# Kernel tuning notes

Measured on AMD Instinct MI355X. Metric: run time of the kernel, lower is better.

The kernel has to match this reference:

```python
import jax, jax.numpy as jnp
import numpy as np

B, T, V, H = 1, 1024, 32000, 2048
NH, NKV, HD = 8, 4, 256
QS, KVS = NH * HD, NKV * HD
I, L = 8192, 2
SCALE = 256.0 ** -0.5          # query_pre_attn_scalar ** -0.5
ATTN_CAP, FINAL_CAP = 50.0, 30.0
WIN, EPS, THETA = 512, 1e-6, 10000.0
NEG = -2.3819763e38


def setup_inputs() -> dict:
    key = jax.random.key(0)
    ks = jax.random.split(key, 12)
    s = 0.02
    return {
        "tokens": jax.random.randint(ks[0], (B, T), 0, V, dtype=jnp.int32),
        "embed": jax.random.normal(ks[1], (V, H), jnp.float32) * s,
        "qkv_w": jax.random.normal(ks[2], (L, (NH + 2 * NKV) * HD, H), jnp.float32) * s,
        "o_w": jax.random.normal(ks[3], (L, H, NH * HD), jnp.float32) * s,
        "gate_w": jax.random.normal(ks[4], (L, I, H), jnp.float32) * s,
        "up_w": jax.random.normal(ks[5], (L, I, H), jnp.float32) * s,
        "down_w": jax.random.normal(ks[6], (L, H, I), jnp.float32) * s,
        "ln_in": jax.random.normal(ks[7], (L, H), jnp.float32) * s,   # RMSNorm weight (zeros-init offset)
        "ln_pa": jax.random.normal(ks[8], (L, H), jnp.float32) * s,
        "ln_pre": jax.random.normal(ks[9], (L, H), jnp.float32) * s,
        "ln_post": jax.random.normal(ks[10], (L, H), jnp.float32) * s,
        "ln_f": jax.random.normal(ks[11], (H,), jnp.float32) * s,
    }


def rmsnorm(x, w):
    x = x.astype(jnp.float32)
    n = x * jax.lax.rsqrt(jnp.mean(x * x, axis=-1, keepdims=True) + EPS)
    return n * (1.0 + w)  # add_unit_offset=True


def rope(x, cos, sin):
    # x: [B, T, N, HD]; split-half complex rotary as in apply_rotary_emb
    x1, x2 = jnp.split(x, 2, axis=-1)
    c = cos[None, :, None, :]
    s = sin[None, :, None, :]
    return jnp.concatenate([x1 * c - x2 * s, x1 * s + x2 * c], axis=-1)


def reference(tokens, embed, qkv_w, o_w, gate_w, up_w, down_w,
              ln_in, ln_pa, ln_pre, ln_post, ln_f):
    pos = jnp.arange(T)
    inv = 1.0 / (THETA ** (jnp.arange(0, HD, 2, dtype=jnp.float32) / HD))  # [HD/2]
    ang = pos.astype(jnp.float32)[:, None] * inv[None, :]
    cos, sin = jnp.cos(ang), jnp.sin(ang)

    i, j = pos[:, None], pos[None, :]
    causal = j <= i
    mask_global = jnp.where(causal, 0.0, NEG).astype(jnp.float32)
    mask_local = jnp.where(causal & (i - j < WIN), 0.0, NEG).astype(jnp.float32)
    masks = [mask_local, mask_global]  # layer 0: LOCAL_SLIDING, layer 1: GLOBAL

    x = embed[tokens] * jnp.sqrt(jnp.float32(H))  # Gemma embedding normalizer

    for l in range(L):
        h = rmsnorm(x, ln_in[l])
        qkv = jnp.einsum('bth,oh->bto', h, qkv_w[l])
        q = qkv[..., :QS].reshape(B, T, NH, HD)
        k = qkv[..., QS:QS + KVS].reshape(B, T, NKV, HD)
        v = qkv[..., QS + KVS:].reshape(B, T, NKV, HD)
        q = rope(q, cos, sin)
        k = rope(k, cos, sin)
        # prefill: kv_write_indices=arange(T) -> cache == current k/v
        k = jnp.repeat(k, NH // NKV, axis=2)  # GQA repeat_interleave over heads
        v = jnp.repeat(v, NH // NKV, axis=2)
        scores = jnp.einsum('bqhd,bkhd->bhqk', q * SCALE, k)
        scores = jnp.tanh(scores / ATTN_CAP) * ATTN_CAP
        scores = scores + masks[l][None, None]
        attn = jax.nn.softmax(scores.astype(jnp.float32), axis=-1)
        out = jnp.einsum('bhqk,bkhd->bqhd', attn, v).reshape(B, T, NH * HD)
        out = jnp.einsum('bto,ho->bth', out, o_w[l])
        x = x + rmsnorm(out, ln_pa[l])

        h = rmsnorm(x, ln_pre[l])
        gate = jax.nn.gelu(jnp.einsum('bth,ih->bti', h, gate_w[l]), approximate=True)
        up = jnp.einsum('bth,ih->bti', h, up_w[l])
        ff = jnp.einsum('bti,hi->bth', gate * up, down_w[l])
        x = x + rmsnorm(ff, ln_post[l])

    x = rmsnorm(x, ln_f)
    logits = jnp.einsum('bth,vh->btv', x, embed)
    logits = jnp.tanh(logits / FINAL_CAP) * FINAL_CAP  # final_logit_softcapping
    return logits
```

## Files before the change

### kernel.cpp

```cpp
#include <hip/hip_runtime.h>
#include <hip/hip_bf16.h>
#include <math.h>

typedef unsigned short u16;
typedef __attribute__((ext_vector_type(8))) short bf16x8;
typedef __attribute__((ext_vector_type(4))) float f32x4;
typedef __attribute__((ext_vector_type(4))) u16 u16x4;
typedef __attribute__((ext_vector_type(4))) unsigned u32x4;

#define T_SEQ 1024
#define HDIM  2048
#define NHEAD 8
#define NKVH  4
#define HSZ   256
#define ISZ   8192
#define NVOC  32000

#define GLDS(src, dst) __builtin_amdgcn_global_load_lds( \
    (const __attribute__((address_space(1))) void*)(src), \
    (__attribute__((address_space(3))) void*)(dst), 16, 0, 0)

__device__ __forceinline__ u16 f2bf(float f) {
    union { float f; unsigned u; } v; v.f = f;
    return (u16)((v.u + 0x7fffu + ((v.u >> 16) & 1u)) >> 16);
}
__device__ __forceinline__ float bf2f(u16 h) {
    union { unsigned u; float f; } v; v.u = (unsigned)h << 16; return v.f;
}

__device__ __forceinline__ unsigned cvt_pk_bf16(float a, float b) {
    unsigned r;
    asm("v_cvt_pk_bf16_f32 %0, %1, %2" : "=v"(r) : "v"(a), "v"(b));
    return r;
}

__device__ __forceinline__ float fast_tanh(float x) {
    float e = __expf(-2.0f * fabsf(x));
    float t = (1.0f - e) / (1.0f + e);
    return copysignf(t, x);
}

__device__ __forceinline__ f32x4 mfma16(bf16x8 a, bf16x8 b, f32x4 c) {
    return __builtin_amdgcn_mfma_f32_16x16x32_bf16(a, b, c, 0, 0, 0);
}

template<int EPI>
__global__ __launch_bounds__(512, 1)
void gemm_f(const u16* __restrict__ A, int lda,
            const float* __restrict__ B, int ldb,
            float* __restrict__ C, int ldc, long sC, int K)
{
    extern __shared__ char lds[];
    const int t = threadIdx.x;
    const int lane = t & 63, wid = t >> 6;
    const int z = blockIdx.z;
    A += (long)z * K;
    B += (long)z * K;
    C += (long)z * sC;

    const int nwg = gridDim.x * gridDim.y;
    int flat = blockIdx.y * gridDim.x + blockIdx.x;
    {
        const int q = nwg >> 3, r = nwg & 7;
        const int xcd = flat & 7, loc = flat >> 3;
        flat = (xcd < r ? xcd * (q + 1) : r * (q + 1) + (xcd - r) * q) + loc;
    }
    const int gm = gridDim.y;
    const long m0 = (long)(flat % gm) * 256;
    const long n0 = (long)(flat / gm) * 128;

    const int ar = t >> 3;
    const int asl = ((t & 7) ^ (ar & 7)) * 8;
    const u16* gA0 = A + (m0 + ar)       * (long)lda + asl;
    const u16* gA1 = A + (m0 + 64 + ar)  * (long)lda + asl;
    const u16* gA2 = A + (m0 + 128 + ar) * (long)lda + asl;
    const u16* gA3 = A + (m0 + 192 + ar) * (long)lda + asl;
    const int br = t >> 4;
    const int bsl = ((t & 15) ^ (br & 15)) * 4;
    const float* gB0 = B + (n0 + br)      * (long)ldb + bsl;
    const float* gB1 = B + (n0 + 32 + br) * (long)ldb + bsl;
    const float* gB2 = B + (n0 + 64 + br) * (long)ldb + bsl;
    const float* gB3 = B + (n0 + 96 + br) * (long)ldb + bsl;

    auto stage = [&](int kt) {
        const long ko = (long)kt * 64;
        char* d = lds + (kt & 1) * 65536 + t * 16;
        GLDS(gA0 + ko, d);
        GLDS(gA1 + ko, d + 8192);
        GLDS(gA2 + ko, d + 16384);
        GLDS(gA3 + ko, d + 24576);
        GLDS(gB0 + ko, d + 32768);
        GLDS(gB1 + ko, d + 40960);
        GLDS(gB2 + ko, d + 49152);
        GLDS(gB3 + ko, d + 57344);
    };

    f32x4 acc[4][4] = {};
    const int fr = lane & 15, kq = lane >> 4;
    const int wm = wid >> 1, wn = wid & 1;
    const int ps0 = ((kq)     ^ (fr & 7)) * 8;
    const int ps1 = ((4 + kq) ^ (fr & 7)) * 8;

    const int KT = K >> 6;
    stage(0);
    stage(1);

    for (int kt = 0; kt < KT; ++kt) {
        if (kt < KT - 1) asm volatile("s_waitcnt vmcnt(8)" ::: "memory");
        else             asm volatile("s_waitcnt vmcnt(0)" ::: "memory");
        __builtin_amdgcn_s_barrier();

        const u16*   As = (const u16*)(lds + (kt & 1) * 65536);
        const float* Bs = (const float*)(lds + (kt & 1) * 65536 + 32768);
        const int arow = wm * 64 + fr;
        const int brow = wn * 64 + fr;

        #pragma unroll
        for (int kk = 0; kk < 2; ++kk) {
            const int ps = kk ? ps1 : ps0;
            const int G = 8 * kk + 2 * kq;
            const int sa = G ^ fr, sb = (G + 1) ^ fr;
            bf16x8 af[4], bfv[4];
            #pragma unroll
            for (int mi = 0; mi < 4; ++mi)
                af[mi] = *(const bf16x8*)(As + (arow + mi * 16) * 64 + ps);
            #pragma unroll
            for (int ni = 0; ni < 4; ++ni) {
                const float* rp = Bs + (brow + ni * 16) * 64;
                f32x4 v0 = *(const f32x4*)(rp + sa * 4);
                f32x4 v1 = *(const f32x4*)(rp + sb * 4);
                u32x4 bw;
                bw.x = cvt_pk_bf16(v0.x, v0.y);
                bw.y = cvt_pk_bf16(v0.z, v0.w);
                bw.z = cvt_pk_bf16(v1.x, v1.y);
                bw.w = cvt_pk_bf16(v1.z, v1.w);
                bfv[ni] = __builtin_bit_cast(bf16x8, bw);
            }
            __builtin_amdgcn_s_setprio(1);
            #pragma unroll
            for (int mi = 0; mi < 4; ++mi)
                #pragma unroll
                for (int ni = 0; ni < 4; ++ni)
                    acc[mi][ni] = mfma16(af[mi], bfv[ni], acc[mi][ni]);
            __builtin_amdgcn_s_setprio(0);
        }
        __builtin_amdgcn_s_barrier();
        if (kt + 2 < KT) stage(kt + 2);
    }

    const int crb = kq * 4, ccol = fr;
    #pragma unroll
    for (int mi = 0; mi < 4; ++mi) {
        #pragma unroll
        for (int rr = 0; rr < 4; ++rr) {
            const long row = m0 + wm * 64 + mi * 16 + crb + rr;
            float* cp = C + row * ldc + n0 + wn * 64 + ccol;
            #pragma unroll
            for (int ni = 0; ni < 4; ++ni) {
                float v = acc[mi][ni][rr];
                if (EPI == 1) v = fast_tanh(v * (1.0f / 30.0f)) * 30.0f;
                cp[ni * 16] = v;
            }
        }
    }
}

template<int EPI, typename CT>
__global__ __launch_bounds__(256)
void gemm_bt(const u16* __restrict__ A, int lda, long sA,
             const u16* __restrict__ B, int ldb, long sB, int bshift,
             CT* __restrict__ C, int ldc, long sC, int K,
             int swin, int tflag)
{
    __shared__ u16 As[128 * 32];
    __shared__ u16 Bs[128 * 32];
    const int tid = threadIdx.x;
    const int lane = tid & 63, wid = tid >> 6;
    const int z = blockIdx.z;
    A += (long)z * sA;
    B += (long)(z >> bshift) * sB;
    C += (long)z * sC;

    const int nwg = gridDim.x * gridDim.y;
    int flat = blockIdx.y * gridDim.x + blockIdx.x;
    {
        const int q = nwg >> 3, r = nwg & 7;
        const int xcd = flat & 7, loc = flat >> 3;
        flat = (xcd < r ? xcd * (q + 1) : r * (q + 1) + (xcd - r) * q) + loc;
    }
    const int gm = gridDim.y;
    const long m0 = (long)(flat % gm) * 128;
    const long n0 = (long)(flat / gm) * 128;

    if (swin > 0) {
        if (n0 > m0 + 127) return;
        if (m0 - (n0 + 127) >= swin) return;
    }
    int klo = 0, khi = K;
    if (tflag > 0) {
        const long hi = m0 + 128;
        if (hi < khi) khi = (int)hi;
        const long lo = m0 - (long)tflag + 1;
        klo = lo > 0 ? (int)(lo & ~31L) : 0;
    }

    f32x4 acc[4][4] = {};

    const int ar = tid >> 2, ac = (tid & 3) * 8;
    const u16* gA0 = A + (m0 + ar) * lda + ac;
    const u16* gB0 = B + (n0 + ar) * (long)ldb + ac;
    const long a64 = 64L * lda, b64 = 64L * ldb;

    const int fr = lane & 15, fk = (lane >> 4) * 8;
    const int wm = (wid >> 1) * 64, wn = (wid & 1) * 64;

    for (int k0 = klo; k0 < khi; k0 += 32) {
        GLDS(gA0 + k0,       &As[tid * 8]);
        GLDS(gA0 + a64 + k0, &As[2048 + tid * 8]);
        GLDS(gB0 + k0,       &Bs[tid * 8]);
        GLDS(gB0 + b64 + k0, &Bs[2048 + tid * 8]);
        __syncthreads();
        bf16x8 af[4], bfv[4];
        #pragma unroll
        for (int mi = 0; mi < 4; ++mi)
            af[mi] = *(const bf16x8*)(&As[(wm + mi * 16 + fr) * 32 + fk]);
        #pragma unroll
        for (int ni = 0; ni < 4; ++ni)
            bfv[ni] = *(const bf16x8*)(&Bs[(wn + ni * 16 + fr) * 32 + fk]);
        #pragma unroll
        for (int mi = 0; mi < 4; ++mi)
            #pragma unroll
            for (int ni = 0; ni < 4; ++ni)
                acc[mi][ni] = mfma16(af[mi], bfv[ni], acc[mi][ni]);
        __syncthreads();
    }

    const int crb = (lane >> 4) * 4, ccol = lane & 15;
    #pragma unroll
    for (int mi = 0; mi < 4; ++mi) {
        #pragma unroll
        for (int rr = 0; rr < 4; ++rr) {
            const long row = m0 + wm + mi * 16 + crb + rr;
            CT* cp = C + row * ldc + n0 + wn + ccol;
            #pragma unroll
            for (int ni = 0; ni < 4; ++ni) {
                float v = acc[mi][ni][rr];
                if (EPI == 1) v = fast_tanh(v * (1.0f / 30.0f)) * 30.0f;
                if constexpr (sizeof(CT) == 2) cp[ni * 16] = f2bf(v);
                else                           cp[ni * 16] = v;
            }
        }
    }
}

__global__ __launch_bounds__(256)
void embed_scale(const int* __restrict__ tok, const float* __restrict__ emb,
                 float* __restrict__ x)
{
    const int t = blockIdx.x, tid = threadIdx.x;
    const long src = (long)tok[t] * HDIM;
    f32x4 a = *(const f32x4*)(emb + src + tid * 8);
    f32x4 b = *(const f32x4*)(emb + src + tid * 8 + 4);
    a *= 45.254834f; b *= 45.254834f;
    *(f32x4*)(x + (long)t * HDIM + tid * 8) = a;
    *(f32x4*)(x + (long)t * HDIM + tid * 8 + 4) = b;
}

__device__ __forceinline__ float block_sum(float v, float* red) {
    #pragma unroll
    for (int o = 32; o; o >>= 1) v += __shfl_xor(v, o);
    const int tid = threadIdx.x;
    if ((tid & 63) == 0) red[tid >> 6] = v;
    __syncthreads();
    return red[0] + red[1] + red[2] + red[3];
}

__global__ __launch_bounds__(256)
void rmsnorm_bf16(const float* __restrict__ x, const float* __restrict__ w,
                  u16* __restrict__ out)
{
    __shared__ float red[4];
    const int t = blockIdx.x, tid = threadIdx.x;
    const float* row = x + (long)t * HDIM;
    f32x4 a = *(const f32x4*)(row + tid * 8);
    f32x4 b = *(const f32x4*)(row + tid * 8 + 4);
    float ss = a.x*a.x + a.y*a.y + a.z*a.z + a.w*a.w
             + b.x*b.x + b.y*b.y + b.z*b.z + b.w*b.w;
    ss = block_sum(ss, red);
    const float r = rsqrtf(ss * (1.0f / HDIM) + 1e-6f);
    f32x4 wa = *(const f32x4*)(w + tid * 8);
    f32x4 wb = *(const f32x4*)(w + tid * 8 + 4);
    u16x4 o0, o1;
    o0.x = f2bf(a.x * r * (1.0f + wa.x)); o0.y = f2bf(a.y * r * (1.0f + wa.y));
    o0.z = f2bf(a.z * r * (1.0f + wa.z)); o0.w = f2bf(a.w * r * (1.0f + wa.w));
    o1.x = f2bf(b.x * r * (1.0f + wb.x)); o1.y = f2bf(b.y * r * (1.0f + wb.y));
    o1.z = f2bf(b.z * r * (1.0f + wb.z)); o1.w = f2bf(b.w * r * (1.0f + wb.w));
    *(u16x4*)(out + (long)t * HDIM + tid * 8) = o0;
    *(u16x4*)(out + (long)t * HDIM + tid * 8 + 4) = o1;
}

__global__ __launch_bounds__(256)
void add_rmsnorm(float* __restrict__ x, const float* __restrict__ y,
                 const float* __restrict__ w, int nsplit, long stride)
{
    __shared__ float red[4];
    const int t = blockIdx.x, tid = threadIdx.x;
    const float* yr = y + (long)t * HDIM;
    f32x4 a = *(const f32x4*)(yr + tid * 8);
    f32x4 b = *(const f32x4*)(yr + tid * 8 + 4);
    for (int s = 1; s < nsplit; ++s) {
        a += *(const f32x4*)(yr + s * stride + tid * 8);
        b += *(const f32x4*)(yr + s * stride + tid * 8 + 4);
    }
    float ss = a.x*a.x + a.y*a.y + a.z*a.z + a.w*a.w
             + b.x*b.x + b.y*b.y + b.z*b.z + b.w*b.w;
    ss = block_sum(ss, red);
    const float r = rsqrtf(ss * (1.0f / HDIM) + 1e-6f);
    f32x4 wa = *(const f32x4*)(w + tid * 8);
    f32x4 wb = *(const f32x4*)(w + tid * 8 + 4);
    float* xr = x + (long)t * HDIM;
    f32x4 xa = *(const f32x4*)(xr + tid * 8);
    f32x4 xb = *(const f32x4*)(xr + tid * 8 + 4);
    xa.x += a.x * r * (1.0f + wa.x); xa.y += a.y * r * (1.0f + wa.y);
    xa.z += a.z * r * (1.0f + wa.z); xa.w += a.w * r * (1.0f + wa.w);
    xb.x += b.x * r * (1.0f + wb.x); xb.y += b.y * r * (1.0f + wb.y);
    xb.z += b.z * r * (1.0f + wb.z); xb.w += b.w * r * (1.0f + wb.w);
    *(f32x4*)(xr + tid * 8) = xa;
    *(f32x4*)(xr + tid * 8 + 4) = xb;
}

#define QKV_STRIDE (1024L * 4096)

__global__ __launch_bounds__(256)
void qkv_post(const float* __restrict__ qkv, u16* __restrict__ qb,
              u16* __restrict__ kb)
{
    const int t = blockIdx.x, tid = threadIdx.x;
    const float* row = qkv + (long)t * 4096;
    const float ft = (float)t;
    #pragma unroll
    for (int it = 0; it < 4; ++it) {
        const int p = tid + it * 256;
        const int nh = p >> 7, d = p & 127;
        const float inv = powf(10000.0f, -(float)d * (1.0f / 128.0f));
        const float ang = ft * inv;
        const float c = cosf(ang), s = sinf(ang);
        const int i1 = nh * 256 + d, i2 = i1 + 128;
        const float x1 = row[i1] + row[i1 + QKV_STRIDE];
        const float x2 = row[i2] + row[i2 + QKV_STRIDE];
        const long ob = ((long)nh * T_SEQ + t) * HSZ;
        qb[ob + d]       = f2bf((x1 * c - x2 * s) * 0.0625f);
        qb[ob + 128 + d] = f2bf((x1 * s + x2 * c) * 0.0625f);
    }
    #pragma unroll
    for (int it = 0; it < 2; ++it) {
        const int p = tid + it * 256;
        const int kv = p >> 7, d = p & 127;
        const float inv = powf(10000.0f, -(float)d * (1.0f / 128.0f));
        const float ang = ft * inv;
        const float c = cosf(ang), s = sinf(ang);
        const int i1 = 2048 + kv * 256 + d, i2 = i1 + 128;
        const float x1 = row[i1] + row[i1 + QKV_STRIDE];
        const float x2 = row[i2] + row[i2 + QKV_STRIDE];
        const long ob = ((long)kv * T_SEQ + t) * HSZ;
        kb[ob + d]       = f2bf(x1 * c - x2 * s);
        kb[ob + 128 + d] = f2bf(x1 * s + x2 * c);
    }
}

__global__ __launch_bounds__(256)
void v_transpose(const float* __restrict__ qkvb, u16* __restrict__ vT)
{
    __shared__ u16 tile[64][65];
    const int t0 = blockIdx.x * 64, d0 = blockIdx.y * 64, kv = blockIdx.z;
    const int lane = threadIdx.x & 63, w = threadIdx.x >> 6;
    #pragma unroll
    for (int i = 0; i < 16; ++i) {
        const int t = w * 16 + i;
        const long idx = (long)(t0 + t) * 4096 + 3072 + kv * 256 + d0 + lane;
        tile[t][lane] = f2bf(qkvb[idx] + qkvb[idx + QKV_STRIDE]);
    }
    __syncthreads();
    #pragma unroll
    for (int i = 0; i < 16; ++i) {
        const int d = w * 16 + i;
        vT[((long)kv * HSZ + d0 + d) * T_SEQ + t0 + lane] = tile[lane][d];
    }
}

__global__ __launch_bounds__(256)
void softmax_mask(const float* __restrict__ sc, u16* __restrict__ pr, int win)
{
    __shared__ float redm[4], reds[4];
    const int i = blockIdx.x, h = blockIdx.y, tid = threadIdx.x;
    const long base = ((long)h * T_SEQ + i) * T_SEQ;
    f32x4 sv = *(const f32x4*)(sc + base + tid * 4);
    float vals[4];
    #pragma unroll
    for (int j = 0; j < 4; ++j) {
        const int col = tid * 4 + j;
        const float s = fast_tanh(sv[j] * 0.02f) * 50.0f;
        const bool valid = (col <= i) && ((i - col) < win);
        vals[j] = valid ? s : -3.0e38f;
    }
    float m = fmaxf(fmaxf(vals[0], vals[1]), fmaxf(vals[2], vals[3]));
    #pragma unroll
    for (int o = 32; o; o >>= 1) m = fmaxf(m, __shfl_xor(m, o));
    if ((tid & 63) == 0) redm[tid >> 6] = m;
    __syncthreads();
    m = fmaxf(fmaxf(redm[0], redm[1]), fmaxf(redm[2], redm[3]));
    float sum = 0.0f;
    #pragma unroll
    for (int j = 0; j < 4; ++j) { vals[j] = __expf(vals[j] - m); sum += vals[j]; }
    #pragma unroll
    for (int o = 32; o; o >>= 1) sum += __shfl_xor(sum, o);
    if ((tid & 63) == 0) reds[tid >> 6] = sum;
    __syncthreads();
    sum = reds[0] + reds[1] + reds[2] + reds[3];
    const float inv = 1.0f / sum;
    u16x4 o4;
    #pragma unroll
    for (int j = 0; j < 4; ++j) o4[j] = f2bf(vals[j] * inv);
    *(u16x4*)(pr + base + tid * 4) = o4;
}

__global__ __launch_bounds__(256)
void mul_gelu(const float* __restrict__ g, const float* __restrict__ u,
              u16* __restrict__ p)
{
    const int n4 = (T_SEQ * ISZ) / 4;
    for (int i = blockIdx.x * 256 + threadIdx.x; i < n4; i += gridDim.x * 256) {
        f32x4 gv = ((const f32x4*)g)[i];
        f32x4 uv = ((const f32x4*)u)[i];
        u16x4 w;
        #pragma unroll
        for (int j = 0; j < 4; ++j) {
            const float xg = gv[j];
            const float tt = fast_tanh(0.79788456f * (xg + 0.044715f * xg * xg * xg));
            w[j] = f2bf(0.5f * xg * (1.0f + tt) * uv[j]);
        }
        ((u16x4*)p)[i] = w;
    }
}

extern "C" void kernel_launch(void* const* d_in, const int* in_sizes, int n_in,
                              void* d_out, int out_size, void* d_ws, size_t ws_size,
                              hipStream_t stream)
{
    (void)in_sizes; (void)n_in; (void)out_size; (void)ws_size;
    const int*   tokens = (const int*)  d_in[0];
    const float* emb    = (const float*)d_in[1];
    const float* qkv_w  = (const float*)d_in[2];
    const float* o_w    = (const float*)d_in[3];
    const float* gate_w = (const float*)d_in[4];
    const float* up_w   = (const float*)d_in[5];
    const float* down_w = (const float*)d_in[6];
    const float* ln_in  = (const float*)d_in[7];
    const float* ln_pa  = (const float*)d_in[8];
    const float* ln_pre = (const float*)d_in[9];
    const float* ln_post= (const float*)d_in[10];
    const float* ln_f   = (const float*)d_in[11];
    float* logits = (float*)d_out;

    char* base = (char*)d_ws;
    size_t off = 0;
    auto alloc = [&](size_t b) { char* p = base + off; off += (b + 255) & ~(size_t)255; return p; };

    float* x    = (float*)alloc((size_t)T_SEQ * HDIM * 4);
    u16*   hb   = (u16*)  alloc((size_t)T_SEQ * HDIM * 2);
    u16*   qb   = (u16*)  alloc((size_t)NHEAD * T_SEQ * HSZ * 2);
    u16*   kb   = (u16*)  alloc((size_t)NKVH * T_SEQ * HSZ * 2);
    u16*   vT   = (u16*)  alloc((size_t)NKVH * HSZ * T_SEQ * 2);
    u16*   ao   = (u16*)  alloc((size_t)T_SEQ * HDIM * 2);
    u16*   pb   = (u16*)  alloc((size_t)T_SEQ * ISZ * 2);
    char*  big  = alloc((size_t)2 * T_SEQ * ISZ * 4);
    float* P    = (float*)big;
    float* sc   = (float*)big;
    u16*   pr   = (u16*)(big + (size_t)NHEAD * T_SEQ * T_SEQ * 4);
    float* gb   = (float*)big;
    float* ub   = (float*)(big + (size_t)T_SEQ * ISZ * 4);

    const size_t LDSF = 2 * 65536;
    const long s2048 = 1024L * 2048;
    const int BIGWIN = 1 << 29;

    embed_scale<<<T_SEQ, 256, 0, stream>>>(tokens, emb, x);
    for (int l = 0; l < 2; ++l) {
        const int win = (l == 0) ? 512 : BIGWIN;
        rmsnorm_bf16<<<T_SEQ, 256, 0, stream>>>(x, ln_in + l * HDIM, hb);
        gemm_f<0><<<dim3(32, 4, 2), 512, LDSF, stream>>>(
            hb, HDIM, qkv_w + (size_t)l * 4096 * HDIM, HDIM, P, 4096, QKV_STRIDE, 1024);
        qkv_post<<<T_SEQ, 256, 0, stream>>>(P, qb, kb);
        v_transpose<<<dim3(16, 4, 4), 256, 0, stream>>>(P, vT);
        gemm_bt<0, float><<<dim3(8, 8, NHEAD), 256, 0, stream>>>(
            qb, HSZ, (long)T_SEQ * HSZ, kb, HSZ, (long)T_SEQ * HSZ, 1,
            sc, T_SEQ, (long)T_SEQ * T_SEQ, HSZ, win, 0);
        softmax_mask<<<dim3(T_SEQ, NHEAD, 1), 256, 0, stream>>>(
            sc, pr, l == 0 ? 512 : (1 << 30));
        gemm_bt<0, u16><<<dim3(2, 8, NHEAD), 256, 0, stream>>>(
            pr, T_SEQ, (long)T_SEQ * T_SEQ, vT, T_SEQ, (long)HSZ * T_SEQ, 1,
            ao, HDIM, (long)HSZ, T_SEQ, 0, win);
        gemm_f<0><<<dim3(16, 4, 4), 512, LDSF, stream>>>(
            ao, HDIM, o_w + (size_t)l * HDIM * HDIM, HDIM, P, HDIM, s2048, 512);
        add_rmsnorm<<<T_SEQ, 256, 0, stream>>>(x, P, ln_pa + l * HDIM, 4, s2048);
        rmsnorm_bf16<<<T_SEQ, 256, 0, stream>>>(x, ln_pre + l * HDIM, hb);
        gemm_f<0><<<dim3(64, 4, 1), 512, LDSF, stream>>>(
            hb, HDIM, gate_w + (size_t)l * ISZ * HDIM, HDIM, gb, ISZ, 0, HDIM);
        gemm_f<0><<<dim3(64, 4, 1), 512, LDSF, stream>>>(
            hb, HDIM, up_w + (size_t)l * ISZ * HDIM, HDIM, ub, ISZ, 0, HDIM);
        mul_gelu<<<2048, 256, 0, stream>>>(gb, ub, pb);
        gemm_f<0><<<dim3(16, 4, 4), 512, LDSF, stream>>>(
            pb, ISZ, down_w + (size_t)l * HDIM * ISZ, ISZ, P, HDIM, s2048, 2048);
        add_rmsnorm<<<T_SEQ, 256, 0, stream>>>(x, P, ln_post + l * HDIM, 4, s2048);
    }
    rmsnorm_bf16<<<T_SEQ, 256, 0, stream>>>(x, ln_f, hb);
    gemm_f<1><<<dim3(250, 4, 1), 512, LDSF, stream>>>(
        hb, HDIM, emb, HDIM, logits, NVOC, 0, HDIM);
}
```

Baseline: 810.0 us.

## Convert fp32 B tile to bf16 once in LDS and fuse GELU-mul into gate GEMM

Each k-step, the GEMM now converts the fp32 weight tile to bf16 once into a separate swizzled LDS buffer. Before, every wave converted the B fragments it read on its own, so the same data was converted by several waves and fp32 LDS reads were doubled. The change also removes the separate mul_gelu kernel: the gate GEMM's epilogue applies tanh-GELU, multiplies by the up-projection output and writes bf16 directly. This drops the fp32 gate buffer's round trip through memory. In exchange it adds an extra barrier and lgkmcnt wait per k-step, and raises LDS use to 144KB.

```diff
diff --git a/kernel.cpp b/kernel.cpp
--- a/kernel.cpp
+++ b/kernel.cpp
@@ -44,11 +44,12 @@
     return __builtin_amdgcn_mfma_f32_16x16x32_bf16(a, b, c, 0, 0, 0);
 }
 
-template<int EPI>
+template<int EPI, typename CT>
 __global__ __launch_bounds__(512, 1)
-void gemm_f(const u16* __restrict__ A, int lda,
+void gemm_c(const u16* __restrict__ A, int lda,
             const float* __restrict__ B, int ldb,
-            float* __restrict__ C, int ldc, long sC, int K)
+            CT* __restrict__ C, int ldc, long sC, int K,
+            const float* __restrict__ UP)
 {
     extern __shared__ char lds[];
     const int t = threadIdx.x;
@@ -101,6 +102,9 @@
     const int ps0 = ((kq)     ^ (fr & 7)) * 8;
     const int ps1 = ((4 + kq) ^ (fr & 7)) * 8;
 
+    const int cr = t & 127, cpair = t >> 7;
+    u16* bdst_base = (u16*)(lds + 131072) + cr * 64;
+
     const int KT = K >> 6;
     stage(0);
     stage(1);
@@ -110,32 +114,38 @@
         else             asm volatile("s_waitcnt vmcnt(0)" ::: "memory");
         __builtin_amdgcn_s_barrier();
 
-        const u16*   As = (const u16*)(lds + (kt & 1) * 65536);
-        const float* Bs = (const float*)(lds + (kt & 1) * 65536 + 32768);
+        {
+            const float* bsrc = (const float*)(lds + (kt & 1) * 65536 + 32768) + cr * 64;
+            #pragma unroll
+            for (int jj = 0; jj < 2; ++jj) {
+                const int j = 2 * cpair + jj;
+                f32x4 v0 = *(const f32x4*)(bsrc + ((2 * j)     ^ (cr & 15)) * 4);
+                f32x4 v1 = *(const f32x4*)(bsrc + ((2 * j + 1) ^ (cr & 15)) * 4);
+                u32x4 w;
+                w.x = cvt_pk_bf16(v0.x, v0.y);
+                w.y = cvt_pk_bf16(v0.z, v0.w);
+                w.z = cvt_pk_bf16(v1.x, v1.y);
+                w.w = cvt_pk_bf16(v1.z, v1.w);
+                *(u32x4*)(bdst_base + (j ^ (cr & 7)) * 8) = w;
+            }
+        }
+        asm volatile("s_waitcnt lgkmcnt(0)" ::: "memory");
+        __builtin_amdgcn_s_barrier();
+
+        const u16* As   = (const u16*)(lds + (kt & 1) * 65536);
+        const u16* Bs16 = (const u16*)(lds + 131072);
         const int arow = wm * 64 + fr;
         const int brow = wn * 64 + fr;
-
         #pragma unroll
         for (int kk = 0; kk < 2; ++kk) {
             const int ps = kk ? ps1 : ps0;
-            const int G = 8 * kk + 2 * kq;
-            const int sa = G ^ fr, sb = (G + 1) ^ fr;
             bf16x8 af[4], bfv[4];
             #pragma unroll
             for (int mi = 0; mi < 4; ++mi)
                 af[mi] = *(const bf16x8*)(As + (arow + mi * 16) * 64 + ps);
             #pragma unroll
-            for (int ni = 0; ni < 4; ++ni) {
-                const float* rp = Bs + (brow + ni * 16) * 64;
-                f32x4 v0 = *(const f32x4*)(rp + sa * 4);
-                f32x4 v1 = *(const f32x4*)(rp + sb * 4);
-                u32x4 bw;
-                bw.x = cvt_pk_bf16(v0.x, v0.y);
-                bw.y = cvt_pk_bf16(v0.z, v0.w);
-                bw.z = cvt_pk_bf16(v1.x, v1.y);
-                bw.w = cvt_pk_bf16(v1.z, v1.w);
-                bfv[ni] = __builtin_bit_cast(bf16x8, bw);
-            }
+            for (int ni = 0; ni < 4; ++ni)
+                bfv[ni] = *(const bf16x8*)(Bs16 + (brow + ni * 16) * 64 + ps);
             __builtin_amdgcn_s_setprio(1);
             #pragma unroll
             for (int mi = 0; mi < 4; ++mi)
@@ -154,12 +164,20 @@
         #pragma unroll
         for (int rr = 0; rr < 4; ++rr) {
             const long row = m0 + wm * 64 + mi * 16 + crb + rr;
-            float* cp = C + row * ldc + n0 + wn * 64 + ccol;
+            CT* cp = C + row * ldc + n0 + wn * 64 + ccol;
+            const float* upp = UP + row * (long)ldc + n0 + wn * 64 + ccol;
             #pragma unroll
             for (int ni = 0; ni < 4; ++ni) {
                 float v = acc[mi][ni][rr];
-                if (EPI == 1) v = fast_tanh(v * (1.0f / 30.0f)) * 30.0f;
-                cp[ni * 16] = v;
+                if (EPI == 1) {
+                    cp[ni * 16] = (CT)(fast_tanh(v * (1.0f / 30.0f)) * 30.0f);
+                } else if (EPI == 2) {
+                    const float tt = fast_tanh(0.79788456f * (v + 0.044715f * v * v * v));
+                    const float g = 0.5f * v * (1.0f + tt);
+                    ((u16*)cp)[ni * 16] = f2bf(g * upp[ni * 16]);
+                } else {
+                    cp[ni * 16] = (CT)v;
+                }
             }
         }
     }
@@ -424,25 +442,6 @@
     *(u16x4*)(pr + base + tid * 4) = o4;
 }
 
-__global__ __launch_bounds__(256)
-void mul_gelu(const float* __restrict__ g, const float* __restrict__ u,
-              u16* __restrict__ p)
-{
-    const int n4 = (T_SEQ * ISZ) / 4;
-    for (int i = blockIdx.x * 256 + threadIdx.x; i < n4; i += gridDim.x * 256) {
-        f32x4 gv = ((const f32x4*)g)[i];
-        f32x4 uv = ((const f32x4*)u)[i];
-        u16x4 w;
-        #pragma unroll
-        for (int j = 0; j < 4; ++j) {
-            const float xg = gv[j];
-            const float tt = fast_tanh(0.79788456f * (xg + 0.044715f * xg * xg * xg));
-            w[j] = f2bf(0.5f * xg * (1.0f + tt) * uv[j]);
-        }
-        ((u16x4*)p)[i] = w;
-    }
-}
-
 extern "C" void kernel_launch(void* const* d_in, const int* in_sizes, int n_in,
                               void* d_out, int out_size, void* d_ws, size_t ws_size,
                               hipStream_t stream)
@@ -477,10 +476,9 @@
     float* P    = (float*)big;
     float* sc   = (float*)big;
     u16*   pr   = (u16*)(big + (size_t)NHEAD * T_SEQ * T_SEQ * 4);
-    float* gb   = (float*)big;
     float* ub   = (float*)(big + (size_t)T_SEQ * ISZ * 4);
 
-    const size_t LDSF = 2 * 65536;
+    const size_t LDSC = 147456;
     const long s2048 = 1024L * 2048;
     const int BIGWIN = 1 << 29;
 
@@ -488,8 +486,8 @@
     for (int l = 0; l < 2; ++l) {
         const int win = (l == 0) ? 512 : BIGWIN;
         rmsnorm_bf16<<<T_SEQ, 256, 0, stream>>>(x, ln_in + l * HDIM, hb);
-        gemm_f<0><<<dim3(32, 4, 2), 512, LDSF, stream>>>(
-            hb, HDIM, qkv_w + (size_t)l * 4096 * HDIM, HDIM, P, 4096, QKV_STRIDE, 1024);
+        gemm_c<0, float><<<dim3(32, 4, 2), 512, LDSC, stream>>>(
+            hb, HDIM, qkv_w + (size_t)l * 4096 * HDIM, HDIM, P, 4096, QKV_STRIDE, 1024, ub);
         qkv_post<<<T_SEQ, 256, 0, stream>>>(P, qb, kb);
         v_transpose<<<dim3(16, 4, 4), 256, 0, stream>>>(P, vT);
         gemm_bt<0, float><<<dim3(8, 8, NHEAD), 256, 0, stream>>>(
@@ -500,20 +498,19 @@
         gemm_bt<0, u16><<<dim3(2, 8, NHEAD), 256, 0, stream>>>(
             pr, T_SEQ, (long)T_SEQ * T_SEQ, vT, T_SEQ, (long)HSZ * T_SEQ, 1,
             ao, HDIM, (long)HSZ, T_SEQ, 0, win);
-        gemm_f<0><<<dim3(16, 4, 4), 512, LDSF, stream>>>(
-            ao, HDIM, o_w + (size_t)l * HDIM * HDIM, HDIM, P, HDIM, s2048, 512);
+        gemm_c<0, float><<<dim3(16, 4, 4), 512, LDSC, stream>>>(
+            ao, HDIM, o_w + (size_t)l * HDIM * HDIM, HDIM, P, HDIM, s2048, 512, ub);
         add_rmsnorm<<<T_SEQ, 256, 0, stream>>>(x, P, ln_pa + l * HDIM, 4, s2048);
         rmsnorm_bf16<<<T_SEQ, 256, 0, stream>>>(x, ln_pre + l * HDIM, hb);
-        gemm_f<0><<<dim3(64, 4, 1), 512, LDSF, stream>>>(
-            hb, HDIM, gate_w + (size_t)l * ISZ * HDIM, HDIM, gb, ISZ, 0, HDIM);
-        gemm_f<0><<<dim3(64, 4, 1), 512, LDSF, stream>>>(
-            hb, HDIM, up_w + (size_t)l * ISZ * HDIM, HDIM, ub, ISZ, 0, HDIM);
-        mul_gelu<<<2048, 256, 0, stream>>>(gb, ub, pb);
-        gemm_f<0><<<dim3(16, 4, 4), 512, LDSF, stream>>>(
-            pb, ISZ, down_w + (size_t)l * HDIM * ISZ, ISZ, P, HDIM, s2048, 2048);
+        gemm_c<0, float><<<dim3(64, 4, 1), 512, LDSC, stream>>>(
+            hb, HDIM, up_w + (size_t)l * ISZ * HDIM, HDIM, ub, ISZ, 0, HDIM, ub);
+        gemm_c<2, u16><<<dim3(64, 4, 1), 512, LDSC, stream>>>(
+            hb, HDIM, gate_w + (size_t)l * ISZ * HDIM, HDIM, pb, ISZ, 0, HDIM, ub);
+        gemm_c<0, float><<<dim3(16, 4, 4), 512, LDSC, stream>>>(
+            pb, ISZ, down_w + (size_t)l * HDIM * ISZ, ISZ, P, HDIM, s2048, 2048, ub);
         add_rmsnorm<<<T_SEQ, 256, 0, stream>>>(x, P, ln_post + l * HDIM, 4, s2048);
     }
     rmsnorm_bf16<<<T_SEQ, 256, 0, stream>>>(x, ln_f, hb);
-    gemm_f<1><<<dim3(250, 4, 1), 512, LDSF, stream>>>(
-        hb, HDIM, emb, HDIM, logits, NVOC, 0, HDIM);
-}
+    gemm_c<1, float><<<dim3(250, 4, 1), 512, LDSC, stream>>>(
+        hb, HDIM, emb, HDIM, logits, NVOC, 0, HDIM, ub);
+}
```

Result: slower. 834.8 us (+3.1%).
